# Kernel tuning notes

Hardware: AMD Instinct MI355X
Metric: run time of the kernel (lower is better)

The kernel has to match this reference:

```python
import jax, jax.numpy as jnp
import numpy as np

B, T, DIM, DIM_EPS, H = 4, 1024, 2048, 2048, 16
HD = DIM // H        # 128, value head dim
HDE = DIM_EPS // H   # 128, q/k head dim


def setup_inputs() -> dict:
    key = jax.random.key(0)
    ks = jax.random.split(key, 6)
    s = 0.02
    # rotary frequencies as in llama-style precompute (theta=10000)
    inv_freq = 1.0 / (10000.0 ** (np.arange(0, HDE, 2, dtype=np.float32) / HDE))
    t = np.arange(T, dtype=np.float32)
    ang = np.outer(t, inv_freq)  # (T, HDE//2)
    return {
        "v": jax.random.normal(ks[0], (B, T, DIM), jnp.float32),
        "x_eps": jax.random.normal(ks[1], (B, T, DIM_EPS), jnp.float32),
        "freqs_cos": jnp.asarray(np.cos(ang)),
        "freqs_sin": jnp.asarray(np.sin(ang)),
        "W_eps_attn": jax.random.normal(ks[2], (DIM_EPS, 2 * DIM_EPS), jnp.float32) * s,
        "W_attn": jax.random.normal(ks[3], (DIM, DIM), jnp.float32) * s,
        "W_proj": jax.random.normal(ks[4], (DIM, DIM), jnp.float32) * s,
        "W_eps_proj": jax.random.normal(ks[5], (DIM_EPS, DIM_EPS), jnp.float32) * s,
    }


def _rope(x, cos, sin):
    # x: (B, T, H, HDE) -> complex-multiply by freqs_cis of shape (T, HDE//2)
    xr = x.reshape(*x.shape[:-1], -1, 2)
    x_re, x_im = xr[..., 0], xr[..., 1]
    c = cos[None, :, None, :]  # (1, T, 1, HDE//2)
    s = sin[None, :, None, :]
    o_re = x_re * c - x_im * s
    o_im = x_re * s + x_im * c
    return jnp.stack([o_re, o_im], axis=-1).reshape(x.shape)


def reference(v, x_eps, freqs_cos, freqs_sin, W_eps_attn, W_attn, W_proj, W_eps_proj):
    Bn, Tn, C = v.shape
    qk = x_eps @ W_eps_attn            # (B, T, 2*DIM_EPS)
    q, k = jnp.split(qk, 2, axis=-1)
    vp = v @ W_attn                    # (B, T, DIM)
    q = _rope(q.reshape(Bn, Tn, H, HDE), freqs_cos, freqs_sin)
    k = _rope(k.reshape(Bn, Tn, H, HDE), freqs_cos, freqs_sin)
    q = q.transpose(0, 2, 1, 3)        # (B, H, T, HDE)
    k = k.transpose(0, 2, 1, 3)
    vh = vp.reshape(Bn, Tn, H, HD).transpose(0, 2, 1, 3)
    scale = 1.0 / jnp.sqrt(jnp.asarray(HDE, q.dtype))
    scores = jnp.einsum("bhqd,bhkd->bhqk", q, k) * scale
    causal = jnp.tril(jnp.ones((Tn, Tn), bool))
    scores = jnp.where(causal[None, None], scores, jnp.finfo(scores.dtype).min)
    att = jax.nn.softmax(scores, axis=-1)
    y = jnp.einsum("bhqk,bhkd->bhqd", att, vh)
    y = y.transpose(0, 2, 1, 3).reshape(Bn, Tn, C)
    v_out = y @ W_proj
    x_eps_out = x_eps @ W_eps_proj
    return (v_out, x_eps_out)
```

## Files before the change

kernel.cpp:

```cpp
#include <hip/hip_runtime.h>
#include <stdint.h>

typedef __attribute__((ext_vector_type(8))) short  short8;
typedef __attribute__((ext_vector_type(4))) float  f32x4;
typedef __attribute__((ext_vector_type(4))) float  float4v;
typedef __attribute__((ext_vector_type(4))) unsigned short ushort4v;
typedef __attribute__((ext_vector_type(4))) unsigned int   u32x4;

#define DEV __device__ __forceinline__

DEV unsigned short f2bf(float f) {
    union { float f; unsigned int u; } x; x.f = f;
    unsigned int u = x.u;
    unsigned int r = (u + 0x7fffu + ((u >> 16) & 1u)) >> 16;
    return (unsigned short)r;
}
DEV float bf2f(unsigned short b) {
    union { unsigned int u; float f; } x; x.u = ((unsigned int)b) << 16;
    return x.f;
}

DEV void gll16(const void* g, void* l) {
    __builtin_amdgcn_global_load_lds(
        (const __attribute__((address_space(1))) void*)g,
        (__attribute__((address_space(3))) void*)l, 16, 0, 0);
}

#define MROWS 4096
#define KDIM  2048
#define NQK   4096

__global__ void prep_kernel(
    const float* __restrict__ xeps, const float* __restrict__ v_in,
    const float* __restrict__ Wea, const float* __restrict__ Wa,
    const float* __restrict__ Wp,  const float* __restrict__ Wep,
    unsigned short* __restrict__ xe16, unsigned short* __restrict__ v16,
    unsigned short* __restrict__ WeaT, unsigned short* __restrict__ WaT,
    unsigned short* __restrict__ WpT,  unsigned short* __restrict__ WepT) {

    __shared__ float tile[32][33];
    const int blk = blockIdx.x, tid = threadIdx.x;

    if (blk < 16384) {
        const float* in = (blk < 8192) ? xeps : v_in;
        unsigned short* out = (blk < 8192) ? xe16 : v16;
        int i = (blk & 8191) * 256 + tid;
        float4v f = ((const float4v*)in)[i];
        ushort4v o;
        o[0] = f2bf(f[0]); o[1] = f2bf(f[1]); o[2] = f2bf(f[2]); o[3] = f2bf(f[3]);
        ((ushort4v*)out)[i] = o;
        return;
    }
    const float* W; unsigned short* Wt; int K, N, local;
    if (blk < 24576)      { W = Wea; Wt = WeaT; K = KDIM; N = NQK;  local = blk - 16384; }
    else if (blk < 28672) { W = Wa;  Wt = WaT;  K = KDIM; N = KDIM; local = blk - 24576; }
    else if (blk < 32768) { W = Wp;  Wt = WpT;  K = KDIM; N = KDIM; local = blk - 28672; }
    else                  { W = Wep; Wt = WepT; K = KDIM; N = KDIM; local = blk - 32768; }
    const int ntiles = N >> 5;
    const int n0 = (local % ntiles) * 32, k0 = (local / ntiles) * 32;
    const int tx = tid & 31, ty = tid >> 5;
#pragma unroll
    for (int j = 0; j < 32; j += 8)
        tile[ty + j][tx] = W[(size_t)(k0 + ty + j) * N + n0 + tx];
    __syncthreads();
#pragma unroll
    for (int j = 0; j < 32; j += 8)
        Wt[(size_t)(n0 + ty + j) * K + k0 + tx] = f2bf(tile[tx][ty + j]);
}

__global__ void add_f32(float* __restrict__ out, const float* __restrict__ add, int n4) {
    int i = blockIdx.x * blockDim.x + threadIdx.x;
    if (i < n4) {
        float4v a = ((const float4v*)out)[i];
        float4v b = ((const float4v*)add)[i];
        a[0] += b[0]; a[1] += b[1]; a[2] += b[2]; a[3] += b[3];
        ((float4v*)out)[i] = a;
    }
}

__global__ __launch_bounds__(512, 2) void gemm256(
    const unsigned short* __restrict__ A0g, const unsigned short* __restrict__ B0g,
    float* __restrict__ Cf0, unsigned short* __restrict__ Ch0,
    int N0, int tx0, int nb0, int outbf0,
    const unsigned short* __restrict__ A1g, const unsigned short* __restrict__ B1g,
    float* __restrict__ Cf1, unsigned short* __restrict__ Ch1,
    int N1, int tx1, int outbf1, int Kst, int Kl,
    const float* __restrict__ rC, const float* __restrict__ rS,
    int mode0, int mode1) {

    __shared__ __align__(16) char lds[131072];

    int blk = blockIdx.x;
    const unsigned short* Ag; const unsigned short* Bg;
    float* Cf; unsigned short* Ch; int N, tx, outbf, nwg, mode;
    if (blk < nb0) { Ag = A0g; Bg = B0g; Cf = Cf0; Ch = Ch0; N = N0; tx = tx0; outbf = outbf0; nwg = nb0; mode = mode0; }
    else { blk -= nb0; Ag = A1g; Bg = B1g; Cf = Cf1; Ch = Ch1; N = N1; tx = tx1; outbf = outbf1; nwg = gridDim.x - nb0; mode = mode1; }
    { int cpx = nwg >> 3; blk = (blk & 7) * cpx + (blk >> 3); }
    const int bx = blk % tx, by = blk / tx;

    const int tid = threadIdx.x;
    const int lane = tid & 63;
    const int w  = tid >> 6;
    const int lr = lane & 15, lk = lane >> 4;
    const int wm = w >> 2, wn = w & 3;
    const int cswz16 = (lk ^ ((lr >> 3) << 1)) * 16;
    const int rdOff  = lr * 64 + cswz16;
    const int bRow0B = (wn & 1) * 4096;

    const unsigned short* Arow = Ag + (size_t)(by * 256) * Kst;
    const unsigned short* Brow = Bg + (size_t)(bx * 256) * Kst;

    const int srow = tid >> 2;
    const int sclog = (tid & 3) ^ (((tid >> 5) & 1) << 1);
    const unsigned short* aSt0 = Arow + (size_t)srow * Kst + sclog * 8;
    const unsigned short* aSt1 = aSt0 + (size_t)128 * Kst;
    const unsigned short* bSt0 = Brow + (size_t)srow * Kst + sclog * 8;
    const unsigned short* bSt1 = bSt0 + (size_t)128 * Kst;

    char* sA0 = lds;            char* sB0 = lds + 32768;
    char* sA1 = lds + 65536;    char* sB1 = lds + 98304;
    const int sOff = tid * 16;

    const char* aB0 = lds + wm * 16384;
    const char* aB1 = aB0 + 65536;
    const char* bB0 = lds + 32768 + (wn >> 1) * 16384;
    const char* bB1 = bB0 + 65536;

    f32x4 acc[8][4];
#pragma unroll
    for (int m = 0; m < 8; ++m)
#pragma unroll
        for (int n = 0; n < 4; ++n) acc[m][n] = (f32x4){0.f, 0.f, 0.f, 0.f};

    const int NT = Kl >> 6;

    auto STAGE = [&](const unsigned short* srcHalf, int k0, char* ldsHalf) {
        gll16(srcHalf + k0,      ldsHalf + sOff);
        gll16(srcHalf + k0 + 32, ldsHalf + 8192 + sOff);
    };

    STAGE(aSt0, 0, sA0);  STAGE(aSt1, 0, sA0 + 16384);
    STAGE(bSt0, 0, sB0);  STAGE(bSt1, 0, sB0 + 16384);
    STAGE(aSt0, 64, sA1);
    asm volatile("s_waitcnt vmcnt(2)" ::: "memory");
    __builtin_amdgcn_s_barrier();

#define MFMA_BF(a, b, c) __builtin_amdgcn_mfma_f32_16x16x32_bf16(a, b, c, 0, 0, 0)

#define RD_A(BASE, MH)                                                               \
    _Pragma("unroll") for (int i = 0; i < 4; ++i) {                                  \
        Ar[i][0] = *(const short8*)((BASE) +        (MH) * 4096 + i * 1024 + rdOff); \
        Ar[i][1] = *(const short8*)((BASE) + 8192 + (MH) * 4096 + i * 1024 + rdOff); \
    }

#define RD_B(BASE, NH)                                                                        \
    _Pragma("unroll") for (int j = 0; j < 2; ++j) {                                           \
        Br[j][0] = *(const short8*)((BASE) +        bRow0B + ((NH) * 2 + j) * 1024 + rdOff);  \
        Br[j][1] = *(const short8*)((BASE) + 8192 + bRow0B + ((NH) * 2 + j) * 1024 + rdOff);  \
    }

#define MFMA16(MH, NH)                                                       \
    __builtin_amdgcn_s_setprio(1);                                           \
    _Pragma("unroll") for (int ks = 0; ks < 2; ++ks)                         \
        _Pragma("unroll") for (int i = 0; i < 4; ++i)                        \
            _Pragma("unroll") for (int j = 0; j < 2; ++j)                    \
                acc[(MH) * 4 + i][(NH) * 2 + j] =                            \
                    MFMA_BF(Ar[i][ks], Br[j][ks], acc[(MH) * 4 + i][(NH) * 2 + j]); \
    __builtin_amdgcn_s_setprio(0);

#define PH(RDS, STG, MFMAQ, VMW)                               \
    {                                                          \
        RDS;                                                   \
        STG;                                                   \
        __builtin_amdgcn_s_barrier();                          \
        asm volatile("s_waitcnt lgkmcnt(0)" ::: "memory");     \
        __builtin_amdgcn_sched_barrier(0);                     \
        MFMAQ;                                                 \
        VMW;                                                   \
        __builtin_amdgcn_s_barrier();                          \
    }

#define VMC2 asm volatile("s_waitcnt vmcnt(2)" ::: "memory")

    short8 Ar[4][2], Br[2][2];

    for (int i2 = 0; i2 < NT; i2 += 2) {
        const int kt1 = (i2 + 1) * 64;
        const int kA  = (i2 + 2 < NT ? i2 + 2 : NT - 1) * 64;
        const int kA3 = (i2 + 3 < NT ? i2 + 3 : NT - 1) * 64;

        PH({ RD_A(aB0, 0) RD_B(bB0, 0) },
           { STAGE(aSt1, kt1, sA1 + 16384); STAGE(bSt0, kt1, sB1); STAGE(bSt1, kt1, sB1 + 16384); },
           MFMA16(0, 0), {})
        PH({ RD_B(bB0, 1) }, {}, MFMA16(0, 1), {})
        PH({ RD_A(aB0, 1) RD_B(bB0, 0) }, {}, MFMA16(1, 0), {})
        PH({ RD_B(bB0, 1) },
           { STAGE(aSt0, kA, sA0); },
           MFMA16(1, 1), VMC2)

        PH({ RD_A(aB1, 0) RD_B(bB1, 0) },
           { STAGE(aSt1, kA, sA0 + 16384); STAGE(bSt0, kA, sB0); STAGE(bSt1, kA, sB0 + 16384); },
           MFMA16(0, 0), {})
        PH({ RD_B(bB1, 1) }, {}, MFMA16(0, 1), {})
        PH({ RD_A(aB1, 1) RD_B(bB1, 0) }, {}, MFMA16(1, 0), {})
        PH({ RD_B(bB1, 1) },
           { STAGE(aSt0, kA3, sA1); },
           MFMA16(1, 1), VMC2)
    }
    asm volatile("s_waitcnt vmcnt(0)" ::: "memory");
#undef RD_A
#undef RD_B
#undef MFMA16
#undef PH
#undef VMC2

    if (outbf) {
        if (mode == 1) {
#pragma unroll
            for (int mf = 0; mf < 8; ++mf)
#pragma unroll
                for (int nf = 0; nf < 4; ++nf)
#pragma unroll
                    for (int r = 0; r < 4; ++r) {
                        int row = by * 256 + wm * 128 + mf * 16 + lk * 4 + r;
                        int col = bx * 256 + wn * 64 + nf * 16 + lr;
                        float val = acc[mf][nf][r];
                        float part = __shfl_xor(val, 1);
                        int t = row & 1023;
                        int i = (col & 127) >> 1;
                        float c = rC[t * 64 + i];
                        float s = rS[t * 64 + i];
                        float o = (lr & 1) ? (part * s + val * c)
                                           : (val * c - part * s);
                        Ch[(size_t)row * N + col] = f2bf(o);
                    }
        } else if (mode == 2) {
#pragma unroll
            for (int mf = 0; mf < 8; ++mf)
#pragma unroll
                for (int nf = 0; nf < 4; ++nf) {
                    int row0 = by * 256 + wm * 128 + mf * 16 + lk * 4;
                    int col  = bx * 256 + wn * 64 + nf * 16 + lr;
                    int b = row0 >> 10, t0 = row0 & 1023;
                    int h = col >> 7,  d  = col & 127;
                    ushort4v o;
#pragma unroll
                    for (int r = 0; r < 4; ++r) o[r] = f2bf(acc[mf][nf][r]);
                    *(ushort4v*)(Ch + (size_t)(b * 16 + h) * 131072
                                    + (size_t)d * 1024 + t0) = o;
                }
        } else {
#pragma unroll
            for (int mf = 0; mf < 8; ++mf)
#pragma unroll
                for (int nf = 0; nf < 4; ++nf)
#pragma unroll
                    for (int r = 0; r < 4; ++r) {
                        int row = by * 256 + wm * 128 + mf * 16 + lk * 4 + r;
                        int col = bx * 256 + wn * 64 + nf * 16 + lr;
                        Ch[(size_t)row * N + col] = f2bf(acc[mf][nf][r]);
                    }
        }
    } else {
#pragma unroll
        for (int mf = 0; mf < 8; ++mf)
#pragma unroll
            for (int nf = 0; nf < 4; ++nf)
#pragma unroll
                for (int r = 0; r < 4; ++r) {
                    int row = by * 256 + wm * 128 + mf * 16 + lk * 4 + r;
                    int col = bx * 256 + wn * 64 + nf * 16 + lr;
                    Cf[(size_t)row * N + col] = acc[mf][nf][r];
                }
    }
}

__global__ __launch_bounds__(256) void attn_kernel(
    const unsigned short* __restrict__ qk,
    const unsigned short* __restrict__ vpT,
    unsigned short* __restrict__ y) {

    const int bh = blockIdx.x;
    const int qt = 7 - (int)blockIdx.y;
    const int b = bh >> 4, h = bh & 15;
    const int qb0 = qt * 128;

    __shared__ __align__(16) unsigned short Kt[64 * 128];
    __shared__ __align__(16) unsigned short Vt[128 * 64];
    __shared__ __align__(16) unsigned short Pl[4 * 32 * 72];

    const int tid = threadIdx.x, w = tid >> 6, lane = tid & 63;
    const int lr = lane & 15, lk = lane >> 4;

    const unsigned short* Qb = qk + (size_t)(b * 1024) * 4096 + h * 128;
    const unsigned short* Kb = Qb + 2048;
    const unsigned short* Vg = vpT + (size_t)bh * 128 * 1024;
    unsigned short* Pw = &Pl[w * 32 * 72];

    short8 qf[2][4];
#pragma unroll
    for (int m = 0; m < 2; ++m) {
        const unsigned short* qrow = Qb + (size_t)(qb0 + w * 32 + m * 16 + lr) * 4096;
#pragma unroll
        for (int db = 0; db < 4; ++db)
            qf[m][db] = *(const short8*)(qrow + db * 32 + lk * 8);
    }

    f32x4 acc[2][8];
#pragma unroll
    for (int m = 0; m < 2; ++m)
#pragma unroll
        for (int n = 0; n < 8; ++n) acc[m][n] = (f32x4){0.f, 0.f, 0.f, 0.f};
    float m_i[2][4], l_i[2][4];
#pragma unroll
    for (int m = 0; m < 2; ++m)
#pragma unroll
        for (int r = 0; r < 4; ++r) { m_i[m][r] = -1e30f; l_i[m][r] = 0.f; }

    const int nkt = 2 * qt + 2;

#pragma unroll
    for (int c = 0; c < 4; ++c) {
        int base = w * 4096 + c * 1024;
        int row  = (base >> 8) + (lane >> 4);
        int scol = ((lane & 15) * 16) ^ ((row & 7) << 4);
        gll16(Kb + (size_t)row * 4096 + (scol >> 1), (char*)Kt + base);
        int d    = (base >> 7) + (lane >> 3);
        int svol = ((lane & 7) * 16) ^ ((d & 7) << 4);
        gll16(Vg + (size_t)d * 1024 + (svol >> 1), (char*)Vt + base);
    }
    __syncthreads();

    u32x4 kreg[4], vreg[4];

    for (int kt = 0; kt < nkt; ++kt) {
        const bool pf = (kt + 1 < nkt);
        if (pf) {
            const int ktn = kt + 1;
#pragma unroll
            for (int c = 0; c < 4; ++c) {
                int base = w * 4096 + c * 1024;
                int row  = (base >> 8) + (lane >> 4);
                int scol = ((lane & 15) * 16) ^ ((row & 7) << 4);
                kreg[c] = *(const u32x4*)(Kb + (size_t)(ktn * 64 + row) * 4096 + (scol >> 1));
                int d    = (base >> 7) + (lane >> 3);
                int svol = ((lane & 7) * 16) ^ ((d & 7) << 4);
                vreg[c] = *(const u32x4*)(Vg + (size_t)d * 1024 + ktn * 64 + (svol >> 1));
            }
        }

        f32x4 s[2][4];
#pragma unroll
        for (int m = 0; m < 2; ++m)
#pragma unroll
            for (int n = 0; n < 4; ++n) s[m][n] = (f32x4){0.f, 0.f, 0.f, 0.f};
#pragma unroll
        for (int db = 0; db < 4; ++db)
#pragma unroll
            for (int n = 0; n < 4; ++n) {
                int krow = n * 16 + lr;
                int cb = (db * 64 + lk * 16) ^ ((krow & 7) << 4);
                short8 kf = *(const short8*)((const char*)Kt + krow * 256 + cb);
                s[0][n] = __builtin_amdgcn_mfma_f32_16x16x32_bf16(qf[0][db], kf, s[0][n], 0, 0, 0);
                s[1][n] = __builtin_amdgcn_mfma_f32_16x16x32_bf16(qf[1][db], kf, s[1][n], 0, 0, 0);
            }

        const float sc = 0.08838834764831845f;
        const bool diag = (kt >= 2 * qt);
#pragma unroll
        for (int m = 0; m < 2; ++m)
#pragma unroll
            for (int n = 0; n < 4; ++n)
#pragma unroll
                for (int r = 0; r < 4; ++r) {
                    float v = s[m][n][r] * sc;
                    if (diag) {
                        int q   = qb0 + w * 32 + m * 16 + lk * 4 + r;
                        int key = kt * 64 + n * 16 + lr;
                        if (key > q) v = -1e30f;
                    }
                    s[m][n][r] = v;
                }

#pragma unroll
        for (int m = 0; m < 2; ++m) {
            float pm[4];
#pragma unroll
            for (int r = 0; r < 4; ++r)
                pm[r] = fmaxf(fmaxf(s[m][0][r], s[m][1][r]), fmaxf(s[m][2][r], s[m][3][r]));
#pragma unroll
            for (int o = 1; o < 16; o <<= 1)
#pragma unroll
                for (int r = 0; r < 4; ++r)
                    pm[r] = fmaxf(pm[r], __shfl_xor(pm[r], o, 16));

            bool small = true;
#pragma unroll
            for (int r = 0; r < 4; ++r)
                small = small && (pm[r] <= m_i[m][r] + 8.0f);
            if (!__all((int)small)) {
                float resc[4];
#pragma unroll
                for (int r = 0; r < 4; ++r) {
                    float mn = fmaxf(m_i[m][r], pm[r]);
                    resc[r] = __expf(m_i[m][r] - mn);
                    m_i[m][r] = mn;
                    l_i[m][r] *= resc[r];
                }
#pragma unroll
                for (int n = 0; n < 8; ++n)
#pragma unroll
                    for (int r = 0; r < 4; ++r)
                        acc[m][n][r] *= resc[r];
            }

            float rs[4] = {0.f, 0.f, 0.f, 0.f};
#pragma unroll
            for (int n = 0; n < 4; ++n)
#pragma unroll
                for (int r = 0; r < 4; ++r) {
                    float p = __expf(s[m][n][r] - m_i[m][r]);
                    s[m][n][r] = p;
                    rs[r] += p;
                }
#pragma unroll
            for (int o = 1; o < 16; o <<= 1)
#pragma unroll
                for (int r = 0; r < 4; ++r)
                    rs[r] += __shfl_xor(rs[r], o, 16);
#pragma unroll
            for (int r = 0; r < 4; ++r)
                l_i[m][r] += rs[r];

#pragma unroll
            for (int n = 0; n < 4; ++n)
#pragma unroll
                for (int r = 0; r < 4; ++r)
                    Pw[(m * 16 + lk * 4 + r) * 72 + n * 16 + lr] = f2bf(s[m][n][r]);
        }

#pragma unroll
        for (int ks = 0; ks < 2; ++ks) {
            short8 pf0 = *(const short8*)&Pw[(lr) * 72 + ks * 32 + lk * 8];
            short8 pf1 = *(const short8*)&Pw[(16 + lr) * 72 + ks * 32 + lk * 8];
#pragma unroll
            for (int n8 = 0; n8 < 8; ++n8) {
                int d  = n8 * 16 + lr;
                int cb = (ks * 64 + lk * 16) ^ ((d & 7) << 4);
                short8 vf = *(const short8*)((const char*)Vt + d * 128 + cb);
                acc[0][n8] = __builtin_amdgcn_mfma_f32_16x16x32_bf16(pf0, vf, acc[0][n8], 0, 0, 0);
                acc[1][n8] = __builtin_amdgcn_mfma_f32_16x16x32_bf16(pf1, vf, acc[1][n8], 0, 0, 0);
            }
        }
        __syncthreads();

        if (pf) {
#pragma unroll
            for (int c = 0; c < 4; ++c) {
                int base = w * 4096 + c * 1024;
                *(u32x4*)((char*)Kt + base + lane * 16) = kreg[c];
                *(u32x4*)((char*)Vt + base + lane * 16) = vreg[c];
            }
        }
        __syncthreads();
    }

    unsigned short* yb = y + (size_t)(b * 1024) * 2048 + h * 128;
#pragma unroll
    for (int m = 0; m < 2; ++m)
#pragma unroll
        for (int n8 = 0; n8 < 8; ++n8)
#pragma unroll
            for (int r = 0; r < 4; ++r) {
                int t = qb0 + w * 32 + m * 16 + lk * 4 + r;
                int d = n8 * 16 + lr;
                yb[(size_t)t * 2048 + d] = f2bf(acc[m][n8][r] / l_i[m][r]);
            }
}

extern "C" void kernel_launch(void* const* d_in, const int* in_sizes, int n_in,
                              void* d_out, int out_size, void* d_ws, size_t ws_size,
                              hipStream_t stream) {
    const float* v_in  = (const float*)d_in[0];
    const float* xeps  = (const float*)d_in[1];
    const float* fcos  = (const float*)d_in[2];
    const float* fsin  = (const float*)d_in[3];
    const float* Wea   = (const float*)d_in[4];
    const float* Wa    = (const float*)d_in[5];
    const float* Wp    = (const float*)d_in[6];
    const float* Wep   = (const float*)d_in[7];
    float* out = (float*)d_out;

    char* ws = (char*)d_ws;
    unsigned short* xe16 = (unsigned short*)ws;  ws += (size_t)MROWS * KDIM * 2;
    unsigned short* v16  = (unsigned short*)ws;  ws += (size_t)MROWS * KDIM * 2;
    unsigned short* WeaT = (unsigned short*)ws;  ws += (size_t)NQK * KDIM * 2;
    unsigned short* WaT  = (unsigned short*)ws;  ws += (size_t)KDIM * KDIM * 2;
    unsigned short* WpT  = (unsigned short*)ws;  ws += (size_t)KDIM * KDIM * 2;
    unsigned short* WepT = (unsigned short*)ws;  ws += (size_t)KDIM * KDIM * 2;
    unsigned short* qk16 = (unsigned short*)ws;  ws += (size_t)MROWS * NQK * 2;
    unsigned short* vpT  = (unsigned short*)ws;  ws += (size_t)MROWS * KDIM * 2;
    unsigned short* y16  = (unsigned short*)ws;  ws += (size_t)MROWS * KDIM * 2;
    float* projP = (float*)qk16;

    prep_kernel<<<36864, 256, 0, stream>>>(xeps, v_in, Wea, Wa, Wp, Wep,
                                           xe16, v16, WeaT, WaT, WpT, WepT);

    gemm256<<<256, 512, 0, stream>>>(
        xe16, WeaT, nullptr, qk16, NQK, 16, 256, 1,
        xe16, WeaT, nullptr, qk16, NQK, 16, 1, KDIM, KDIM,
        fcos, fsin, 1, 1);

    gemm256<<<256, 512, 0, stream>>>(
        v16,  WaT,  nullptr, vpT, KDIM, 8, 128, 1,
        xe16, WepT, out + (size_t)MROWS * KDIM, nullptr, KDIM, 8, 0, KDIM, KDIM,
        fcos, fsin, 2, 0);

    attn_kernel<<<dim3(64, 8), 256, 0, stream>>>(qk16, vpT, y16);

    gemm256<<<256, 512, 0, stream>>>(
        y16,        WpT,        out,   nullptr, KDIM, 8, 128, 0,
        y16 + 1024, WpT + 1024, projP, nullptr, KDIM, 8, 0, KDIM, 1024,
        fcos, fsin, 0, 0);

    add_f32<<<8192, 256, 0, stream>>>(out, projP, MROWS * KDIM / 4);
}
```

Baseline: 300.1 us.

## Replace split-K output projection and add pass with a 128x256 tile GEMM

The final y@W_proj projection used to run as a split-K gemm256 with two K halves, writing a partial into a scratch buffer and summing it with a separate add kernel. It now runs a new gemm128 kernel with 128x256 tiles over the full K, giving 256 workgroups with no split. That removes the extra fp32 partial write and read and one kernel launch. The trade-off is a K loop twice as long per workgroup and a different staging schedule, plus an XCD-aware remap of block indices.

```diff
diff --git a/kernel.cpp b/kernel.cpp
--- a/kernel.cpp
+++ b/kernel.cpp
@@ -66,16 +66,6 @@
 #pragma unroll
     for (int j = 0; j < 32; j += 8)
         Wt[(size_t)(n0 + ty + j) * K + k0 + tx] = f2bf(tile[tx][ty + j]);
-}
-
-__global__ void add_f32(float* __restrict__ out, const float* __restrict__ add, int n4) {
-    int i = blockIdx.x * blockDim.x + threadIdx.x;
-    if (i < n4) {
-        float4v a = ((const float4v*)out)[i];
-        float4v b = ((const float4v*)add)[i];
-        a[0] += b[0]; a[1] += b[1]; a[2] += b[2]; a[3] += b[3];
-        ((float4v*)out)[i] = a;
-    }
 }
 
 __global__ __launch_bounds__(512, 2) void gemm256(
@@ -275,6 +265,129 @@
     }
 }
 
+__global__ __launch_bounds__(512) void gemm128(
+    const unsigned short* __restrict__ Ag, const unsigned short* __restrict__ Bg,
+    float* __restrict__ Cf, int N, int tx, int Kst) {
+
+    __shared__ __align__(16) char lds[98304];
+
+    int blk = blockIdx.x;
+    { int cpx = (int)gridDim.x >> 3; blk = (blk & 7) * cpx + (blk >> 3); }
+    const int bx = blk % tx, by = blk / tx;
+
+    const int tid = threadIdx.x;
+    const int lane = tid & 63;
+    const int w  = tid >> 6;
+    const int lr = lane & 15, lk = lane >> 4;
+    const int wm = w >> 2, wn = w & 3;
+    const int cswz16 = (lk ^ ((lr >> 3) << 1)) * 16;
+    const int rdOff  = lr * 64 + cswz16;
+    const int bRow0B = (wn & 1) * 4096;
+
+    const unsigned short* Arow = Ag + (size_t)(by * 128) * Kst;
+    const unsigned short* Brow = Bg + (size_t)(bx * 256) * Kst;
+
+    const int srow = tid >> 2;
+    const int sclog = (tid & 3) ^ (((tid >> 5) & 1) << 1);
+    const unsigned short* aSt  = Arow + (size_t)srow * Kst + sclog * 8;
+    const unsigned short* bSt0 = Brow + (size_t)srow * Kst + sclog * 8;
+    const unsigned short* bSt1 = bSt0 + (size_t)128 * Kst;
+
+    const int sOff = tid * 16;
+
+    f32x4 acc[4][4];
+#pragma unroll
+    for (int m = 0; m < 4; ++m)
+#pragma unroll
+        for (int n = 0; n < 4; ++n) acc[m][n] = (f32x4){0.f, 0.f, 0.f, 0.f};
+
+    const int NT = Kst >> 6;
+
+    auto STAGE = [&](const unsigned short* srcHalf, int k0, char* ldsHalf) {
+        gll16(srcHalf + k0,      ldsHalf + sOff);
+        gll16(srcHalf + k0 + 32, ldsHalf + 8192 + sOff);
+    };
+
+#define MFMA_BF(a, b, c) __builtin_amdgcn_mfma_f32_16x16x32_bf16(a, b, c, 0, 0, 0)
+
+    STAGE(aSt,  0,  lds);
+    STAGE(bSt0, 0,  lds + 16384);  STAGE(bSt1, 0, lds + 32768);
+    STAGE(aSt,  64, lds + 49152);
+    asm volatile("s_waitcnt vmcnt(2)" ::: "memory");
+    __builtin_amdgcn_s_barrier();
+
+    short8 Ar[4][2], Br[2][2];
+
+    for (int t = 0; t < NT; ++t) {
+        const int par = t & 1;
+        const char* aW = lds + (par ? 49152 : 0) + wm * 4096;
+        const char* bC = lds + (par ? 65536 : 16384) + (wn >> 1) * 16384;
+        char* dB = lds + (par ? 16384 : 65536);
+        char* dA = lds + (par ? 49152 : 0);
+        const int kB  = (t + 1 < NT ? t + 1 : NT - 1) * 64;
+        const int kA2 = (t + 2 < NT ? t + 2 : NT - 1) * 64;
+
+#pragma unroll
+        for (int i = 0; i < 4; ++i) {
+            Ar[i][0] = *(const short8*)(aW +        i * 1024 + rdOff);
+            Ar[i][1] = *(const short8*)(aW + 8192 + i * 1024 + rdOff);
+        }
+#pragma unroll
+        for (int j = 0; j < 2; ++j) {
+            Br[j][0] = *(const short8*)(bC +        bRow0B + j * 1024 + rdOff);
+            Br[j][1] = *(const short8*)(bC + 8192 + bRow0B + j * 1024 + rdOff);
+        }
+        STAGE(bSt0, kB, dB);  STAGE(bSt1, kB, dB + 16384);
+        __builtin_amdgcn_s_barrier();
+        asm volatile("s_waitcnt lgkmcnt(0)" ::: "memory");
+        __builtin_amdgcn_sched_barrier(0);
+        __builtin_amdgcn_s_setprio(1);
+#pragma unroll
+        for (int ks = 0; ks < 2; ++ks)
+#pragma unroll
+            for (int i = 0; i < 4; ++i)
+#pragma unroll
+                for (int j = 0; j < 2; ++j)
+                    acc[i][j] = MFMA_BF(Ar[i][ks], Br[j][ks], acc[i][j]);
+        __builtin_amdgcn_s_setprio(0);
+        __builtin_amdgcn_s_barrier();
+
+#pragma unroll
+        for (int j = 0; j < 2; ++j) {
+            Br[j][0] = *(const short8*)(bC +        bRow0B + (2 + j) * 1024 + rdOff);
+            Br[j][1] = *(const short8*)(bC + 8192 + bRow0B + (2 + j) * 1024 + rdOff);
+        }
+        STAGE(aSt, kA2, dA);
+        __builtin_amdgcn_s_barrier();
+        asm volatile("s_waitcnt lgkmcnt(0)" ::: "memory");
+        __builtin_amdgcn_sched_barrier(0);
+        __builtin_amdgcn_s_setprio(1);
+#pragma unroll
+        for (int ks = 0; ks < 2; ++ks)
+#pragma unroll
+            for (int i = 0; i < 4; ++i)
+#pragma unroll
+                for (int j = 0; j < 2; ++j)
+                    acc[i][2 + j] = MFMA_BF(Ar[i][ks], Br[j][ks], acc[i][2 + j]);
+        __builtin_amdgcn_s_setprio(0);
+        asm volatile("s_waitcnt vmcnt(2)" ::: "memory");
+        __builtin_amdgcn_s_barrier();
+    }
+    asm volatile("s_waitcnt vmcnt(0)" ::: "memory");
+#undef MFMA_BF
+
+#pragma unroll
+    for (int mf = 0; mf < 4; ++mf)
+#pragma unroll
+        for (int nf = 0; nf < 4; ++nf)
+#pragma unroll
+            for (int r = 0; r < 4; ++r) {
+                int row = by * 128 + wm * 64 + mf * 16 + lk * 4 + r;
+                int col = bx * 256 + wn * 64 + nf * 16 + lr;
+                Cf[(size_t)row * N + col] = acc[mf][nf][r];
+            }
+}
+
 __global__ __launch_bounds__(256) void attn_kernel(
     const unsigned short* __restrict__ qk,
     const unsigned short* __restrict__ vpT,
@@ -501,7 +614,6 @@
     unsigned short* qk16 = (unsigned short*)ws;  ws += (size_t)MROWS * NQK * 2;
     unsigned short* vpT  = (unsigned short*)ws;  ws += (size_t)MROWS * KDIM * 2;
     unsigned short* y16  = (unsigned short*)ws;  ws += (size_t)MROWS * KDIM * 2;
-    float* projP = (float*)qk16;
 
     prep_kernel<<<36864, 256, 0, stream>>>(xeps, v_in, Wea, Wa, Wp, Wep,
                                            xe16, v16, WeaT, WaT, WpT, WepT);
@@ -518,10 +630,5 @@
 
     attn_kernel<<<dim3(64, 8), 256, 0, stream>>>(qk16, vpT, y16);
 
-    gemm256<<<256, 512, 0, stream>>>(
-        y16,        WpT,        out,   nullptr, KDIM, 8, 128, 0,
-        y16 + 1024, WpT + 1024, projP, nullptr, KDIM, 8, 0, KDIM, 1024,
-        fcos, fsin, 0, 0);
-
-    add_f32<<<8192, 256, 0, stream>>>(out, projP, MROWS * KDIM / 4);
-}
+    gemm128<<<256, 512, 0, stream>>>(y16, WpT, out, KDIM, 8, KDIM);
+}
```

Measured after the change: 282.3 us. 1.06x faster.
